# Kernel optimization log

Hardware: AMD Instinct MI355X
Metric: run time of the kernel (lower is better)

Reference implementation:

```python
import jax, jax.numpy as jnp
import numpy as np

K = 9          # neighbors (module default k=9, dilation=1 -> plain top-k)
COUT = 256     # out_channels
BN_EPS = 1e-5


def setup_inputs() -> dict:
    key = jax.random.key(0)
    k1, k2 = jax.random.split(key, 2)
    x = jax.random.normal(k1, (8, 128, 2048, 1), jnp.float32)          # [B,C,N,1]
    W = jax.random.normal(k2, (COUT, 2 * 128), jnp.float32) * 0.05     # 1x1 conv weight [Cout, 2C]
    gamma = jnp.ones((COUT,), jnp.float32)                             # BN affine scale
    beta = jnp.zeros((COUT,), jnp.float32)                             # BN affine shift
    return {"x": x, "W": W, "gamma": gamma, "beta": beta}


def reference(x, W, gamma, beta):
    # x: [B, C, N, 1] channels-first point features
    xt = jnp.transpose(x[..., 0], (0, 2, 1))                           # [B, N, C]
    B, N, C = xt.shape

    # --- dense KNN graph (matrix form): squared euclidean distance, k nearest ---
    sq = jnp.sum(xt * xt, axis=-1)                                     # [B, N]
    dist = sq[:, :, None] - 2.0 * jnp.einsum('bnc,bmc->bnm', xt, xt) + sq[:, None, :]
    _, nn_idx = jax.lax.top_k(-dist, K)                                # [B, N, K] neighbor indices

    # --- EdgeConv gather: x_i = center, x_j = neighbor ---
    x_j = jax.vmap(lambda f, i: f[i])(xt, nn_idx)                      # [B, N, K, C]
    x_i = xt[:, :, None, :]                                            # [B, N, 1, C]
    feat = jnp.concatenate(
        [jnp.broadcast_to(x_i, (B, N, K, C)), x_j - x_i], axis=-1)     # [B, N, K, 2C]

    # --- 1x1 conv (no bias) as GEMM over channel dim ---
    h = jnp.einsum('bnkc,oc->bnko', feat, W)                           # [B, N, K, Cout]

    # --- BatchNorm2d (training-mode batch stats over B,N,K per channel) ---
    mean = jnp.mean(h, axis=(0, 1, 2))
    var = jnp.var(h, axis=(0, 1, 2))
    hn = (h - mean) * jax.lax.rsqrt(var + BN_EPS) * gamma + beta

    # --- ReLU then max over k neighbors ---
    out = jnp.max(jax.nn.relu(hn), axis=2)                             # [B, N, Cout]
    return jnp.transpose(out, (0, 2, 1))                               # [B, Cout, N]
```

## Files before the change

### kernel.cpp

```cpp
#include <hip/hip_runtime.h>
#include <float.h>
#include <math.h>

#define BATCH 8
#define CHN   128
#define NPTS  2048
#define KNN   9
#define NOUT  256
#define TOTCNT (BATCH*NPTS*KNN)

typedef __attribute__((ext_vector_type(8))) short short8;
typedef __attribute__((ext_vector_type(4))) float f32x4;

__device__ __forceinline__ unsigned short f2bf(float f) {
    unsigned int u = __float_as_uint(f);
    unsigned int r = (u + 0x7FFFu + ((u >> 16) & 1u)) >> 16;
    return (unsigned short)r;
}
__device__ __forceinline__ float bf2f(unsigned short h) {
    return __uint_as_float(((unsigned int)h) << 16);
}

__global__ __launch_bounds__(256) void prep_kernel(const float* __restrict__ x,
                                                   const float* __restrict__ W,
                                                   unsigned short* __restrict__ xhi,
                                                   unsigned short* __restrict__ xlo,
                                                   unsigned short* __restrict__ whi,
                                                   unsigned short* __restrict__ wlo,
                                                   float* __restrict__ sqh,
                                                   float* __restrict__ stats) {
    __shared__ float xt[128 * 65];
    __shared__ float psq[256];
    const int b = blockIdx.x, tid = threadIdx.x;
    if (blockIdx.y == 32) {
        stats[b * 512 + tid] = 0.f;
        stats[b * 512 + 256 + tid] = 0.f;
#pragma unroll
        for (int e = 0; e < 32; ++e) {
            int idx = e * 256 + tid;
            int r = b * 64 + (idx >> 7), c = idx & 127;
            float v = (r < 256) ? (W[r * 256 + c] - W[r * 256 + 128 + c])
                                : W[(r - 256) * 256 + 128 + c];
            unsigned short h = f2bf(v);
            float hf = bf2f(h);
            whi[r * 128 + c] = h;
            wlo[r * 128 + c] = f2bf(v - hf);
        }
        return;
    }
    const int n0 = blockIdx.y * 64;
#pragma unroll 4
    for (int p = 0; p < 32; ++p) {
        int c = p * 4 + (tid >> 6), n = tid & 63;
        xt[c * 65 + n] = x[((size_t)b * CHN + c) * NPTS + n0 + n];
    }
    __syncthreads();
    const int n = tid >> 2, cq = tid & 3;
    size_t row = (size_t)(b * NPTS + n0 + n) * CHN;
    float s = 0.f;
#pragma unroll 8
    for (int j = 0; j < 32; ++j) {
        int c = cq * 32 + j;
        float f = xt[c * 65 + n];
        unsigned short h = f2bf(f);
        float hf = bf2f(h);
        unsigned short l = f2bf(f - hf);
        xhi[row + c] = h;
        xlo[row + c] = l;
        s += f * f;
    }
    psq[tid] = s;
    __syncthreads();
    if (tid < 64)
        sqh[b * NPTS + n0 + tid] =
            0.5f * (psq[tid*4] + psq[tid*4+1] + psq[tid*4+2] + psq[tid*4+3]);
}

__global__ __launch_bounds__(256) void knnpq_mfma(const unsigned short* __restrict__ xhi,
                                                  const unsigned short* __restrict__ xlo,
                                                  const float* __restrict__ sqh,
                                                  const unsigned short* __restrict__ whi,
                                                  const unsigned short* __restrict__ wlo,
                                                  float* __restrict__ pd,
                                                  int* __restrict__ pi,
                                                  float* __restrict__ p,
                                                  unsigned short* __restrict__ q) {
    __shared__ __align__(16) unsigned short aS[16384];

    const int tid = threadIdx.x;
    const int b  = blockIdx.x;
    const int zr = blockIdx.z;
    const int sub = zr >> 1;
    const int wv = tid >> 6, lane = tid & 63;
    const int quad = lane >> 4, col = lane & 15;
    const int koff = quad * 8;
    const size_t xb = (size_t)b * NPTS * CHN;

    if (zr & 1) {
        const int nt = blockIdx.y >> 2;
        const int ot = ((blockIdx.y & 3) << 2) | sub;
        const int nbase = nt * 256 + wv * 64;
        const int obase = ot * 32;

        f32x4 acc[4][2];
#pragma unroll
        for (int i = 0; i < 4; ++i)
#pragma unroll
            for (int j = 0; j < 2; ++j) acc[i][j] = (f32x4)0.f;

        for (int chk = 0; chk < 4; ++chk) {
            short8 ah[4], al[4];
#pragma unroll
            for (int i = 0; i < 4; ++i) {
                size_t g = xb + (size_t)(nbase + i * 16 + col) * CHN + chk * 32 + koff;
                ah[i] = *(const short8*)&xhi[g];
                al[i] = *(const short8*)&xlo[g];
            }
#pragma unroll
            for (int j = 0; j < 2; ++j) {
                size_t g = (size_t)(obase + j * 16 + col) * CHN + chk * 32 + koff;
                short8 bh = *(const short8*)&whi[g];
                short8 bl = *(const short8*)&wlo[g];
#pragma unroll
                for (int i = 0; i < 4; ++i) {
                    acc[i][j] = __builtin_amdgcn_mfma_f32_16x16x32_bf16(ah[i], bh, acc[i][j], 0, 0, 0);
                    acc[i][j] = __builtin_amdgcn_mfma_f32_16x16x32_bf16(ah[i], bl, acc[i][j], 0, 0, 0);
                    acc[i][j] = __builtin_amdgcn_mfma_f32_16x16x32_bf16(al[i], bh, acc[i][j], 0, 0, 0);
                }
            }
        }
#pragma unroll
        for (int i = 0; i < 4; ++i)
#pragma unroll
            for (int j = 0; j < 2; ++j) {
                int oc = (obase + j * 16 + col) & 255;
#pragma unroll
                for (int r = 0; r < 4; ++r) {
                    int n = nbase + i * 16 + quad * 4 + r;
                    size_t off = (size_t)(b * NPTS + n) * NOUT + oc;
                    if (ot < 8) p[off] = acc[i][j][r];
                    else        q[off] = f2bf(acc[i][j][r]);
                }
            }
        return;
    }

    const int q0 = blockIdx.y * 64, ms = sub;
    const int msbase = ms * 512;
    const int myq = q0 + wv * 16 + col;

    short8 qh[4], ql[4];
    {
        const unsigned short* qrh = xhi + xb + (size_t)myq * CHN + koff;
        const unsigned short* qrl = xlo + xb + (size_t)myq * CHN + koff;
#pragma unroll
        for (int chk = 0; chk < 4; ++chk) {
            qh[chk] = *(const short8*)(qrh + chk * 32);
            ql[chk] = *(const short8*)(qrl + chk * 32);
        }
    }

    float dl[KNN]; int il[KNN];
#pragma unroll
    for (int k = 0; k < KNN; ++k) { dl[k] = FLT_MAX; il[k] = 0; }

    auto ins = [&](float v, int idx) {
        if (v < dl[KNN - 1]) {
            bool c0b = v < dl[0];
#pragma unroll
            for (int k = KNN - 1; k >= 1; --k) {
                bool sh   = v < dl[k - 1];
                bool here = v < dl[k];
                float nd = sh ? dl[k - 1] : (here ? v : dl[k]);
                int   ni = sh ? il[k - 1] : (here ? idx : il[k]);
                dl[k] = nd; il[k] = ni;
            }
            if (c0b) { dl[0] = v; il[0] = idx; }
        }
    };
    auto ins2 = [&](float v, int idx) {
        if ((v < dl[KNN - 1]) || (v == dl[KNN - 1] && idx < il[KNN - 1])) {
            bool c0b = (v < dl[0]) || (v == dl[0] && idx < il[0]);
#pragma unroll
            for (int k = KNN - 1; k >= 1; --k) {
                bool sh   = (v < dl[k - 1]) || (v == dl[k - 1] && idx < il[k - 1]);
                bool here = (v < dl[k])     || (v == dl[k]     && idx < il[k]);
                float nd = sh ? dl[k - 1] : (here ? v : dl[k]);
                int   ni = sh ? il[k - 1] : (here ? idx : il[k]);
                dl[k] = nd; il[k] = ni;
            }
            if (c0b) { dl[0] = v; il[0] = idx; }
        }
    };

    const unsigned short* gsrc[4];
    {
        const int rA = tid >> 4;
        const int sc8 = ((tid & 15) ^ rA) << 3;
#pragma unroll
        for (int t = 0; t < 4; ++t) {
            const unsigned short* pl = (t >= 2) ? xlo : xhi;
            gsrc[t] = pl + xb + (size_t)(msbase + ((t & 1) << 4) + rA) * CHN + sc8;
        }
    }
    short8 stv[4];
    auto stage_load = [&](int ch) {
#pragma unroll
        for (int t = 0; t < 4; ++t)
            stv[t] = *(const short8*)(gsrc[t] + (size_t)ch * (32 * CHN));
    };
    auto stage_write = [&](int bf) {
        char* d = (char*)aS + bf * 16384 + tid * 16;
#pragma unroll
        for (int t = 0; t < 4; ++t)
            *(short8*)(d + t * 4096) = stv[t];
    };

    const int rowb = col << 8;
    int cofs[4];
#pragma unroll
    for (int chk = 0; chk < 4; ++chk)
        cofs[chk] = (((chk << 2) | quad) ^ col) << 4;
    const float* smb = sqh + b * NPTS + msbase + quad * 4;

    stage_load(0);
    stage_write(0);
    stage_load(1);
    __syncthreads();

    int buf = 0;
    for (int ch = 0; ch < 16; ++ch) {
        if (ch < 15) stage_write(buf ^ 1);
        if (ch < 14) stage_load(ch + 2);

        const char* ab = (const char*)aS + buf * 16384;
        float4 s0 = *(const float4*)(smb + ch * 32);
        float4 s1 = *(const float4*)(smb + ch * 32 + 16);

        f32x4 acc[2];
        acc[0] = (f32x4)0.f; acc[1] = (f32x4)0.f;
#pragma unroll
        for (int chk = 0; chk < 4; ++chk) {
            short8 mh0 = *(const short8*)(ab + rowb + cofs[chk]);
            short8 mh1 = *(const short8*)(ab + 4096 + rowb + cofs[chk]);
            short8 ml0 = *(const short8*)(ab + 8192 + rowb + cofs[chk]);
            short8 ml1 = *(const short8*)(ab + 12288 + rowb + cofs[chk]);
            acc[0] = __builtin_amdgcn_mfma_f32_16x16x32_bf16(mh0, qh[chk], acc[0], 0, 0, 0);
            acc[0] = __builtin_amdgcn_mfma_f32_16x16x32_bf16(mh0, ql[chk], acc[0], 0, 0, 0);
            acc[0] = __builtin_amdgcn_mfma_f32_16x16x32_bf16(ml0, qh[chk], acc[0], 0, 0, 0);
            acc[1] = __builtin_amdgcn_mfma_f32_16x16x32_bf16(mh1, qh[chk], acc[1], 0, 0, 0);
            acc[1] = __builtin_amdgcn_mfma_f32_16x16x32_bf16(mh1, ql[chk], acc[1], 0, 0, 0);
            acc[1] = __builtin_amdgcn_mfma_f32_16x16x32_bf16(ml1, qh[chk], acc[1], 0, 0, 0);
        }

        {
            float d0 = s0.x - acc[0][0], d1 = s0.y - acc[0][1];
            float d2 = s0.z - acc[0][2], d3 = s0.w - acc[0][3];
            float mn4 = fminf(fminf(d0, d1), fminf(d2, d3));
            if (mn4 < dl[KNN - 1]) {
                int ib = msbase + ch * 32 + quad * 4;
                ins(d0, ib); ins(d1, ib + 1); ins(d2, ib + 2); ins(d3, ib + 3);
            }
            d0 = s1.x - acc[1][0]; d1 = s1.y - acc[1][1];
            d2 = s1.z - acc[1][2]; d3 = s1.w - acc[1][3];
            mn4 = fminf(fminf(d0, d1), fminf(d2, d3));
            if (mn4 < dl[KNN - 1]) {
                int ib = msbase + ch * 32 + 16 + quad * 4;
                ins(d0, ib); ins(d1, ib + 1); ins(d2, ib + 2); ins(d3, ib + 3);
            }
        }
        __syncthreads();
        buf ^= 1;
    }

#pragma unroll
    for (int rd = 0; rd < 2; ++rd) {
        const int xm = 16 << rd;
        float pv[KNN]; int pix[KNN];
#pragma unroll
        for (int k = 0; k < KNN; ++k) {
            pv[k]  = __shfl_xor(dl[k], xm, 64);
            pix[k] = __shfl_xor(il[k], xm, 64);
        }
#pragma unroll
        for (int k = 0; k < KNN; ++k) ins2(pv[k], pix[k]);
    }

    if (quad == 0) {
        size_t ob = ((size_t)(b * NPTS + myq) * 4 + ms) * KNN;
#pragma unroll
        for (int k = 0; k < KNN; ++k) {
            pd[ob + k] = dl[k];
            pi[ob + k] = il[k];
        }
    }
}

__global__ __launch_bounds__(512) void stats2_kernel(const float* __restrict__ p,
                                                     const unsigned short* __restrict__ q,
                                                     const float* __restrict__ pd,
                                                     const int* __restrict__ pi,
                                                     float* __restrict__ stats,
                                                     unsigned int* __restrict__ hmm) {
    __shared__ int idx_s[16 * KNN];
    const int b = blockIdx.x, n0 = blockIdx.y * 16;
    const int tid = threadIdx.x;
    const int o = tid & 255, half = tid >> 8;
    if (tid < 16) {
        size_t g = (size_t)(b * NPTS + n0 + tid) * 36;
        const float* d = pd + g;
        const int*   i = pi + g;
        int p0 = 0, p1 = 0, p2 = 0, p3 = 0;
#pragma unroll
        for (int k = 0; k < KNN; ++k) {
            float v0 = (p0 < KNN) ? d[p0]      : FLT_MAX;
            float v1 = (p1 < KNN) ? d[9 + p1]  : FLT_MAX;
            float v2 = (p2 < KNN) ? d[18 + p2] : FLT_MAX;
            float v3 = (p3 < KNN) ? d[27 + p3] : FLT_MAX;
            float best = v0; int sel = 0;
            if (v1 < best) { best = v1; sel = 1; }
            if (v2 < best) { best = v2; sel = 2; }
            if (v3 < best) { best = v3; sel = 3; }
            int idx;
            if      (sel == 0) { idx = i[p0];      p0++; }
            else if (sel == 1) { idx = i[9 + p1];  p1++; }
            else if (sel == 2) { idx = i[18 + p2]; p2++; }
            else               { idx = i[27 + p3]; p3++; }
            idx_s[tid * KNN + k] = idx;
        }
    }
    __syncthreads();
    const unsigned short* qb = q + (size_t)b * NPTS * NOUT + o;
    float s = 0.f, ss = 0.f;
    const int qbase = half * 8;
    for (int qq = 0; qq < 8; qq += 2) {
        const int qi = qbase + qq;
        size_t off0 = (size_t)(b * NPTS + n0 + qi) * NOUT + o;
        size_t off1 = off0 + NOUT;
        float pv0 = p[off0], pv1 = p[off1];
        float h0[KNN], h1[KNN];
#pragma unroll
        for (int k = 0; k < KNN; ++k)
            h0[k] = bf2f(qb[(size_t)idx_s[qi * KNN + k] * NOUT]);
#pragma unroll
        for (int k = 0; k < KNN; ++k)
            h1[k] = bf2f(qb[(size_t)idx_s[(qi + 1) * KNN + k] * NOUT]);
        float mx0 = -FLT_MAX, mn0 = FLT_MAX, mx1 = -FLT_MAX, mn1 = FLT_MAX;
#pragma unroll
        for (int k = 0; k < KNN; ++k) {
            float a = pv0 + h0[k], c = pv1 + h1[k];
            s += a + c; ss += a * a + c * c;
            mx0 = fmaxf(mx0, a); mn0 = fminf(mn0, a);
            mx1 = fmaxf(mx1, c); mn1 = fminf(mn1, c);
        }
        hmm[off0] = ((unsigned int)f2bf(mx0) << 16) | f2bf(mn0);
        hmm[off1] = ((unsigned int)f2bf(mx1) << 16) | f2bf(mn1);
    }
    atomicAdd(&stats[b * 512 + o], s);
    atomicAdd(&stats[b * 512 + NOUT + o], ss);
}

__global__ __launch_bounds__(512) void final_kernel(const unsigned int* __restrict__ hmm,
                                                    const float* __restrict__ stats,
                                                    const float* __restrict__ gamma,
                                                    const float* __restrict__ beta,
                                                    float* __restrict__ out) {
    __shared__ float tr[256 * 17];
    const int b = blockIdx.x, n0 = blockIdx.y * 16;
    const int tid = threadIdx.x;
    const int o = tid & 255, qh = tid >> 8;
    float sum = 0.f, sumsq = 0.f;
#pragma unroll
    for (int i = 0; i < 8; ++i) {
        sum   += stats[i * 512 + o];
        sumsq += stats[i * 512 + NOUT + o];
    }
    const float inv = 1.f / (float)TOTCNT;
    float mean = sum * inv;
    float var  = sumsq * inv - mean * mean;
    float g    = gamma[o] / sqrtf(var + 1e-5f);
    float bet  = beta[o];
    const bool pos = (g >= 0.f);
#pragma unroll
    for (int qq = 0; qq < 8; ++qq) {
        const int qi = qh * 8 + qq;
        size_t off = (size_t)(b * NPTS + n0 + qi) * NOUT + o;
        unsigned int w = hmm[off];
        float v = bf2f(pos ? (unsigned short)(w >> 16) : (unsigned short)(w & 0xFFFFu));
        float hn = (v - mean) * g + bet;
        tr[o * 17 + qi] = fmaxf(hn, 0.f);
    }
    __syncthreads();
    int oo = tid >> 4, qq = tid & 15;
    for (int pass = 0; pass < 8; ++pass) {
        int o_ = pass * 32 + oo;
        out[((size_t)b * NOUT + o_) * NPTS + n0 + qq] = tr[o_ * 17 + qq];
    }
}

extern "C" void kernel_launch(void* const* d_in, const int* in_sizes, int n_in,
                              void* d_out, int out_size, void* d_ws, size_t ws_size,
                              hipStream_t stream) {
    (void)in_sizes; (void)n_in; (void)out_size; (void)ws_size;
    const float* x     = (const float*)d_in[0];
    const float* W     = (const float*)d_in[1];
    const float* gamma = (const float*)d_in[2];
    const float* beta  = (const float*)d_in[3];
    float* out = (float*)d_out;

    char* ws = (char*)d_ws;
    float*          p     = (float*)ws;
    unsigned short* q     = (unsigned short*)(ws + (16u << 20));
    unsigned short* xhi   = (unsigned short*)(ws + (24u << 20));
    unsigned short* xlo   = (unsigned short*)(ws + (28u << 20));
    unsigned int*   hmm   = (unsigned int*)(ws + (32u << 20));
    unsigned short* whi   = (unsigned short*)(ws + (48u << 20));
    unsigned short* wlo   = (unsigned short*)(ws + (48u << 20) + 131072);
    float*          pd    = (float*)(ws + (49u << 20));
    int*            pi    = (int*)  (ws + (52u << 20));
    float*          sqh   = (float*)(ws + (55u << 20));
    float*          stats = (float*)(ws + (55u << 20) + 65536);

    prep_kernel  <<<dim3(8, 33),    256, 0, stream>>>(x, W, xhi, xlo, whi, wlo, sqh, stats);
    knnpq_mfma   <<<dim3(8, 32, 8), 256, 0, stream>>>(xhi, xlo, sqh, whi, wlo, pd, pi, p, q);
    stats2_kernel<<<dim3(8, 128),   512, 0, stream>>>(p, q, pd, pi, stats, hmm);
    final_kernel <<<dim3(8, 128),   512, 0, stream>>>(hmm, stats, gamma, beta, out);
}
```

Measured before the change: 209.5 us.

## Share the KNN pruning threshold across quads and double the block size

```diff
diff --git a/kernel.cpp b/kernel.cpp
--- a/kernel.cpp
+++ b/kernel.cpp
@@ -76,7 +76,7 @@
             0.5f * (psq[tid*4] + psq[tid*4+1] + psq[tid*4+2] + psq[tid*4+3]);
 }
 
-__global__ __launch_bounds__(256) void knnpq_mfma(const unsigned short* __restrict__ xhi,
+__global__ __launch_bounds__(512) void knnpq_mfma(const unsigned short* __restrict__ xhi,
                                                   const unsigned short* __restrict__ xlo,
                                                   const float* __restrict__ sqh,
                                                   const unsigned short* __restrict__ whi,
@@ -97,9 +97,10 @@
     const size_t xb = (size_t)b * NPTS * CHN;
 
     if (zr & 1) {
-        const int nt = blockIdx.y >> 2;
-        const int ot = ((blockIdx.y & 3) << 2) | sub;
-        const int nbase = nt * 256 + wv * 64;
+        const int nt = blockIdx.y >> 1;
+        const int ot = ((blockIdx.y & 1) << 3) | (sub << 1) | (wv >> 2);
+        const int w4 = wv & 3;
+        const int nbase = nt * 256 + w4 * 64;
         const int obase = ot * 32;
 
         f32x4 acc[4][2];
@@ -145,7 +146,7 @@
         return;
     }
 
-    const int q0 = blockIdx.y * 64, ms = sub;
+    const int q0 = blockIdx.y * 128, ms = sub;
     const int msbase = ms * 512;
     const int myq = q0 + wv * 16 + col;
 
@@ -163,20 +164,19 @@
     float dl[KNN]; int il[KNN];
 #pragma unroll
     for (int k = 0; k < KNN; ++k) { dl[k] = FLT_MAX; il[k] = 0; }
-
-    auto ins = [&](float v, int idx) {
-        if (v < dl[KNN - 1]) {
-            bool c0b = v < dl[0];
-#pragma unroll
-            for (int k = KNN - 1; k >= 1; --k) {
-                bool sh   = v < dl[k - 1];
-                bool here = v < dl[k];
-                float nd = sh ? dl[k - 1] : (here ? v : dl[k]);
-                int   ni = sh ? il[k - 1] : (here ? idx : il[k]);
-                dl[k] = nd; il[k] = ni;
-            }
-            if (c0b) { dl[0] = v; il[0] = idx; }
-        }
+    float thr = FLT_MAX;
+
+    auto ins_nochk = [&](float v, int idx) {
+        bool c0b = v < dl[0];
+#pragma unroll
+        for (int k = KNN - 1; k >= 1; --k) {
+            bool sh   = v < dl[k - 1];
+            bool here = v < dl[k];
+            float nd = sh ? dl[k - 1] : (here ? v : dl[k]);
+            int   ni = sh ? il[k - 1] : (here ? idx : il[k]);
+            dl[k] = nd; il[k] = ni;
+        }
+        if (c0b) { dl[0] = v; il[0] = idx; }
     };
     auto ins2 = [&](float v, int idx) {
         if ((v < dl[KNN - 1]) || (v == dl[KNN - 1] && idx < il[KNN - 1])) {
@@ -193,27 +193,22 @@
         }
     };
 
-    const unsigned short* gsrc[4];
+    const unsigned short* gsrc[2];
     {
         const int rA = tid >> 4;
-        const int sc8 = ((tid & 15) ^ rA) << 3;
-#pragma unroll
-        for (int t = 0; t < 4; ++t) {
-            const unsigned short* pl = (t >= 2) ? xlo : xhi;
-            gsrc[t] = pl + xb + (size_t)(msbase + ((t & 1) << 4) + rA) * CHN + sc8;
-        }
-    }
-    short8 stv[4];
+        const int sc8 = ((tid & 15) ^ (rA & 15)) << 3;
+        gsrc[0] = xhi + xb + (size_t)(msbase + rA) * CHN + sc8;
+        gsrc[1] = xlo + xb + (size_t)(msbase + rA) * CHN + sc8;
+    }
+    short8 stv[2];
     auto stage_load = [&](int ch) {
-#pragma unroll
-        for (int t = 0; t < 4; ++t)
-            stv[t] = *(const short8*)(gsrc[t] + (size_t)ch * (32 * CHN));
+        stv[0] = *(const short8*)(gsrc[0] + (size_t)ch * (32 * CHN));
+        stv[1] = *(const short8*)(gsrc[1] + (size_t)ch * (32 * CHN));
     };
     auto stage_write = [&](int bf) {
         char* d = (char*)aS + bf * 16384 + tid * 16;
-#pragma unroll
-        for (int t = 0; t < 4; ++t)
-            *(short8*)(d + t * 4096) = stv[t];
+        *(short8*)(d)        = stv[0];
+        *(short8*)(d + 8192) = stv[1];
     };
 
     const int rowb = col << 8;
@@ -253,22 +248,40 @@
             acc[1] = __builtin_amdgcn_mfma_f32_16x16x32_bf16(ml1, qh[chk], acc[1], 0, 0, 0);
         }
 
+        const int ib = msbase + (ch << 5) + (quad << 2);
+        float d0 = s0.x - acc[0][0], d1 = s0.y - acc[0][1];
+        float d2 = s0.z - acc[0][2], d3 = s0.w - acc[0][3];
+        float d4 = s1.x - acc[1][0], d5 = s1.y - acc[1][1];
+        float d6 = s1.z - acc[1][2], d7 = s1.w - acc[1][3];
+
+        for (;;) {
+            float m01 = fminf(d0, d1); int i01 = (d1 < d0) ? 1  : 0;
+            float m23 = fminf(d2, d3); int i23 = (d3 < d2) ? 3  : 2;
+            float m45 = fminf(d4, d5); int i45 = (d5 < d4) ? 17 : 16;
+            float m67 = fminf(d6, d7); int i67 = (d7 < d6) ? 19 : 18;
+            float mA  = fminf(m01, m23); int iA = (m23 < m01) ? i23 : i01;
+            float mB  = fminf(m45, m67); int iB = (m67 < m45) ? i67 : i45;
+            float mv  = fminf(mA, mB);   int mi = (mB < mA)   ? iB  : iA;
+            bool pass = mv < thr;
+            if (!__any(pass)) break;
+            if (pass) ins_nochk(mv, ib + mi);
+            thr = fminf(thr, dl[KNN - 1]);
+            d0 = (mi == 0)  ? FLT_MAX : d0;
+            d1 = (mi == 1)  ? FLT_MAX : d1;
+            d2 = (mi == 2)  ? FLT_MAX : d2;
+            d3 = (mi == 3)  ? FLT_MAX : d3;
+            d4 = (mi == 16) ? FLT_MAX : d4;
+            d5 = (mi == 17) ? FLT_MAX : d5;
+            d6 = (mi == 18) ? FLT_MAX : d6;
+            d7 = (mi == 19) ? FLT_MAX : d7;
+        }
+
         {
-            float d0 = s0.x - acc[0][0], d1 = s0.y - acc[0][1];
-            float d2 = s0.z - acc[0][2], d3 = s0.w - acc[0][3];
-            float mn4 = fminf(fminf(d0, d1), fminf(d2, d3));
-            if (mn4 < dl[KNN - 1]) {
-                int ib = msbase + ch * 32 + quad * 4;
-                ins(d0, ib); ins(d1, ib + 1); ins(d2, ib + 2); ins(d3, ib + 3);
-            }
-            d0 = s1.x - acc[1][0]; d1 = s1.y - acc[1][1];
-            d2 = s1.z - acc[1][2]; d3 = s1.w - acc[1][3];
-            mn4 = fminf(fminf(d0, d1), fminf(d2, d3));
-            if (mn4 < dl[KNN - 1]) {
-                int ib = msbase + ch * 32 + 16 + quad * 4;
-                ins(d0, ib); ins(d1, ib + 1); ins(d2, ib + 2); ins(d3, ib + 3);
-            }
-        }
+            float t = fminf(dl[KNN - 1], __shfl_xor(dl[KNN - 1], 16, 64));
+            t = fminf(t, __shfl_xor(t, 32, 64));
+            thr = fminf(thr, t);
+        }
+
         __syncthreads();
         buf ^= 1;
     }
@@ -422,7 +435,7 @@
     float*          stats = (float*)(ws + (55u << 20) + 65536);
 
     prep_kernel  <<<dim3(8, 33),    256, 0, stream>>>(x, W, xhi, xlo, whi, wlo, sqh, stats);
-    knnpq_mfma   <<<dim3(8, 32, 8), 256, 0, stream>>>(xhi, xlo, sqh, whi, wlo, pd, pi, p, q);
+    knnpq_mfma   <<<dim3(8, 16, 8), 512, 0, stream>>>(xhi, xlo, sqh, whi, wlo, pd, pi, p, q);
     stats2_kernel<<<dim3(8, 128),   512, 0, stream>>>(p, q, pd, pi, stats, hmm);
     final_kernel <<<dim3(8, 128),   512, 0, stream>>>(hmm, stats, gamma, beta, out);
 }
```

Measured after the change: 216.0 us. +3.1%, slower.
